# Kernel tuning notes

Hardware: AMD Instinct MI355X
Metric: run time of the kernel (lower is better)

Reference implementation:

```python
import jax, jax.numpy as jnp
import numpy as np

N_NODES = 50000
D_IN = 128
HIDDEN = 128
UNITS_DENSE = 256
N_EDGES = 600000
N_PRED = 200000
N_SEL = 300000


def setup_inputs() -> dict:
    key = jax.random.key(0)
    ks = jax.random.split(key, 12)
    node_state = jax.random.normal(ks[0], (N_NODES, D_IN), jnp.float32)
    edge_index = jax.random.randint(ks[1], (2, N_EDGES), 0, N_NODES, jnp.int32)
    out_edges = jax.random.randint(ks[2], (2, N_PRED), 0, N_NODES, jnp.int32)
    set_idx = jnp.sort(jax.random.randint(ks[3], (N_SEL,), 0, 2 * N_PRED, jnp.int32))
    # Glorot-ish scaled weights
    W1 = jax.random.normal(ks[4], (D_IN, HIDDEN), jnp.float32) / np.float32(np.sqrt(D_IN))
    b1 = jnp.zeros((HIDDEN,), jnp.float32)
    W2 = jax.random.normal(ks[5], (HIDDEN, HIDDEN), jnp.float32) / np.float32(np.sqrt(HIDDEN))
    b2 = jnp.zeros((HIDDEN,), jnp.float32)
    dense_W = jax.random.normal(ks[6], (2 * 0 + HIDDEN, UNITS_DENSE), jnp.float32) / np.float32(np.sqrt(HIDDEN))
    dense_b = jnp.zeros((UNITS_DENSE,), jnp.float32)
    out_W = jax.random.normal(ks[7], (UNITS_DENSE, 2), jnp.float32) / np.float32(np.sqrt(UNITS_DENSE))
    out_b = jnp.zeros((2,), jnp.float32)
    return {
        "node_state": node_state, "edge_index": edge_index, "out_edges": out_edges,
        "set_idx": set_idx, "W1": W1, "b1": b1, "W2": W2, "b2": b2,
        "dense_W": dense_W, "dense_b": dense_b, "out_W": out_W, "out_b": out_b,
    }


def _graph_conv(h, src, dst, W, b):
    """DGL GraphConv, norm='both', no activation: D_in^{-1/2} A D_out^{-1/2} H W + b."""
    n = h.shape[0]
    ones = jnp.ones(src.shape[0], h.dtype)
    deg_out = jnp.clip(jax.ops.segment_sum(ones, src, num_segments=n), 1.0)  # [N]
    deg_in = jnp.clip(jax.ops.segment_sum(ones, dst, num_segments=n), 1.0)   # [N]
    h = (h * jax.lax.rsqrt(deg_out)[:, None]) @ W                            # [N, H]
    agg = jax.ops.segment_sum(h[src], dst, num_segments=n)                   # [N, H]
    return agg * jax.lax.rsqrt(deg_in)[:, None] + b


def reference(node_state, edge_index, out_edges, set_idx,
              W1, b1, W2, b2, dense_W, dense_b, out_W, out_b):
    src, dst = edge_index[0], edge_index[1]
    h = _graph_conv(node_state, src, dst, W1, b1)
    h = _graph_conv(h, src, dst, W2, b2)
    # concat along axis=0 as in the original: [2*E_pred, H]
    edge_state = jnp.concatenate([h[out_edges[0]], h[out_edges[1]]], axis=0)
    # boolean_mask replaced by equivalent gather of selected (True) rows
    edge_state_set = edge_state[set_idx]                                      # [N_SEL, H]
    hidden = jax.nn.relu(edge_state_set @ dense_W + dense_b)
    return jax.nn.softmax(hidden @ out_W + out_b, axis=-1)
```

## Files before the change

### kernel.cpp

```cpp
#include <hip/hip_runtime.h>

#define NN 50000
#define DD 128
#define NE 600000
#define NP 200000
#define NS 300000
#define NU 256
#define NBH 64
#define EPB 9375
#define NW 12500
#define NB64 782

typedef __attribute__((ext_vector_type(8))) short short8;
typedef __attribute__((ext_vector_type(4))) float floatx4;

__device__ inline float bf2f(unsigned int u16) {
    unsigned int x = u16 << 16;
    float f; __builtin_memcpy(&f, &x, 4); return f;
}
__device__ inline unsigned short f2bf(float f) {
    unsigned int x; __builtin_memcpy(&x, &f, 4);
    unsigned int lsb = (x >> 16) & 1u;
    x += 0x7fffu + lsb;
    return (unsigned short)(x >> 16);
}

__global__ __launch_bounds__(256) void k_hist(const int* __restrict__ ei,
                                              unsigned int* __restrict__ P) {
    __shared__ unsigned int hw[NW];
    int b = blockIdx.x, half = blockIdx.y, tid = threadIdx.x;
    for (int w = tid; w < NW; w += 256) hw[w] = 0;
    __syncthreads();
    const int* src = ei + (size_t)half * NE;
    int e0 = b * EPB, e1 = min(e0 + EPB, NE);
    for (int e = e0 + tid; e < e1; e += 256) {
        int s = src[e];
        atomicAdd(&hw[s >> 2], 1u << ((s & 3) * 8));
    }
    __syncthreads();
    unsigned int* Pb = P + ((size_t)half * NBH + b) * NW;
    for (int w = tid; w < NW; w += 256) Pb[w] = hw[w];
}

__global__ void k_reduce_cast(const unsigned int* __restrict__ P, int* __restrict__ deg_in,
                              float* __restrict__ r,
                              const float* __restrict__ W1, const float* __restrict__ W2,
                              const float* __restrict__ dW, unsigned short* __restrict__ BT1,
                              unsigned short* __restrict__ BT2, unsigned short* __restrict__ BTd) {
    int gid = blockIdx.x * 256 + threadIdx.x;
    if (gid < 2 * NW) {
        int half = (gid >= NW);
        int wl = gid - half * NW;
        const unsigned int* Ph = P + (size_t)half * NBH * NW + wl;
        int c0 = 0, c1 = 0, c2 = 0, c3 = 0;
        for (int b = 0; b < NBH; ++b) {
            unsigned int v = Ph[(size_t)b * NW];
            c0 += v & 0xff; c1 += (v >> 8) & 0xff; c2 += (v >> 16) & 0xff; c3 += v >> 24;
        }
        int nb = wl * 4;
        if (half) {
            int4 d = {c0, c1, c2, c3};
            *(int4*)(deg_in + nb) = d;
        }
        float4 rr = {rsqrtf((float)max(c0, 1)), rsqrtf((float)max(c1, 1)),
                     rsqrtf((float)max(c2, 1)), rsqrtf((float)max(c3, 1))};
        *(float4*)(r + (size_t)half * NN + nb) = rr;
    }
    {
        int t = gid;
        if (t < 16384) { int rr = t >> 7, cc = t & 127; BT1[cc * 128 + rr] = f2bf(W1[t]); }
        else if (t < 32768) { int t2 = t - 16384; int rr = t2 >> 7, cc = t2 & 127; BT2[cc * 128 + rr] = f2bf(W2[t2]); }
        else if (t < 65536) { int t2 = t - 32768; int rr = t2 >> 8, cc = t2 & 255; BTd[cc * 128 + rr] = f2bf(dW[t2]); }
    }
}

__global__ __launch_bounds__(1024) void k_scan(const int* __restrict__ deg_in,
                                               int* __restrict__ row_ptr) {
    __shared__ int wsum[16];
    __shared__ int woff[16];
    __shared__ int carry_s;
    __shared__ int total_s;
    int tid = threadIdx.x, lane = tid & 63, w = tid >> 6;
    if (tid == 0) carry_s = 0;
    __syncthreads();
    for (int wb = 0; wb < NW; wb += 1024) {
        int i4 = wb + tid;
        int4 v = {0, 0, 0, 0};
        if (i4 < NW) v = *(const int4*)(deg_in + i4 * 4);
        int t0 = v.x, t1 = t0 + v.y, t2 = t1 + v.z, tot = t2 + v.w;
        int x = tot;
#pragma unroll
        for (int off = 1; off < 64; off <<= 1) {
            int y = __shfl_up(x, off);
            if (lane >= off) x += y;
        }
        if (lane == 63) wsum[w] = x;
        __syncthreads();
        if (w == 0 && lane < 16) {
            int s = wsum[lane];
            int xs = s;
#pragma unroll
            for (int off = 1; off < 16; off <<= 1) {
                int y = __shfl_up(xs, off);
                if (lane >= off) xs += y;
            }
            woff[lane] = xs - s;
            if (lane == 15) total_s = xs;
        }
        __syncthreads();
        if (i4 < NW) {
            int base = carry_s + woff[w] + x - tot;
            int4 o = {base, base + t0, base + t1, base + t2};
            *(int4*)(row_ptr + i4 * 4) = o;
        }
        __syncthreads();
        if (tid == 0) carry_s += total_s;
        __syncthreads();
    }
    if (tid == 0) row_ptr[NN] = NE;
}

__global__ void k_colscan(const unsigned int* __restrict__ Pin,
                          unsigned char* __restrict__ baseb) {
    int n = blockIdx.x * 256 + threadIdx.x;
    if (n >= NN) return;
    int wl = n >> 2, sh = (n & 3) * 8;
    int run = 0;
    for (int b = 0; b < NBH; ++b) {
        baseb[(size_t)b * NN + n] = (unsigned char)run;
        run += (Pin[(size_t)b * NW + wl] >> sh) & 0xff;
    }
}

__global__ __launch_bounds__(256) void k_bucket2(const int* __restrict__ ei,
                                                 const int* __restrict__ row_ptr,
                                                 const unsigned char* __restrict__ baseb,
                                                 int* __restrict__ col) {
    __shared__ unsigned int cw[NW];
    int b = blockIdx.x, tid = threadIdx.x;
    for (int w = tid; w < NW; w += 256) cw[w] = 0;
    __syncthreads();
    const unsigned char* bt = baseb + (size_t)b * NN;
    int e0 = b * EPB, e1 = min(e0 + EPB, NE);
    for (int e = e0 + tid; e < e1; e += 256) {
        int s = ei[e], d = ei[NE + e];
        int sh = (d & 3) * 8;
        unsigned int old = atomicAdd(&cw[d >> 2], 1u << sh);
        int local = (old >> sh) & 0xff;
        col[row_ptr[d] + (int)bt[d] + local] = s;
    }
}

template <bool ABF>
__global__ __launch_bounds__(256) void k_gemm_bf(const void* __restrict__ Ap,
                                                 const float* __restrict__ rs,
                                                 const unsigned short* __restrict__ BT,
                                                 unsigned short* __restrict__ Cm) {
    __shared__ unsigned short As[64][136];
    __shared__ unsigned short Bs[128][136];
    int tid = threadIdx.x, lane = tid & 63, wave = tid >> 6;
    int quad = lane >> 4, l16 = lane & 15;
    int row0 = blockIdx.x * 64;

    if (ABF) {
        const unsigned short* A = (const unsigned short*)Ap;
#pragma unroll
        for (int p = 0; p < 4; ++p) {
            int fid = tid + p * 256;
            int r = fid >> 4, c = fid & 15;
            int gr = row0 + r; if (gr > NN - 1) gr = NN - 1;
            *(uint4*)&As[r][c * 8] = *(const uint4*)(A + (size_t)gr * DD + c * 8);
        }
    } else {
        const float* A = (const float*)Ap;
#pragma unroll
        for (int p = 0; p < 8; ++p) {
            int fid = tid + p * 256;
            int r = fid >> 5, c = fid & 31;
            int gr = row0 + r; if (gr > NN - 1) gr = NN - 1;
            float4 v = *(const float4*)(A + (size_t)gr * DD + c * 4);
            ushort4 u;
            u.x = f2bf(v.x); u.y = f2bf(v.y); u.z = f2bf(v.z); u.w = f2bf(v.w);
            *(ushort4*)&As[r][c * 4] = u;
        }
    }
#pragma unroll
    for (int p = 0; p < 8; ++p) {
        int fid = tid + p * 256;
        int r = fid >> 4, c = fid & 15;
        *(uint4*)&Bs[r][c * 8] = *(const uint4*)(BT + (size_t)r * DD + c * 8);
    }
    __syncthreads();

    short8 af[4];
#pragma unroll
    for (int ks = 0; ks < 4; ++ks)
        af[ks] = *(const short8*)&As[wave * 16 + l16][ks * 32 + quad * 8];
    floatx4 acc[8];
#pragma unroll
    for (int nt = 0; nt < 8; ++nt) acc[nt] = (floatx4){0.f, 0.f, 0.f, 0.f};
#pragma unroll
    for (int ks = 0; ks < 4; ++ks) {
#pragma unroll
        for (int nt = 0; nt < 8; ++nt) {
            short8 bf = *(const short8*)&Bs[nt * 16 + l16][ks * 32 + quad * 8];
            acc[nt] = __builtin_amdgcn_mfma_f32_16x16x32_bf16(af[ks], bf, acc[nt], 0, 0, 0);
        }
    }
    int rbase = row0 + wave * 16 + quad * 4;
#pragma unroll
    for (int r = 0; r < 4; ++r) {
        int gr = rbase + r;
        if (gr < NN) {
            float s = rs[gr];
#pragma unroll
            for (int nt = 0; nt < 8; ++nt)
                Cm[(size_t)gr * DD + nt * 16 + l16] = f2bf(acc[nt][r] * s);
        }
    }
}

__global__ __launch_bounds__(256) void k_aggregate(const unsigned short* __restrict__ T,
                                                   const int* __restrict__ row_ptr,
                                                   const int* __restrict__ col,
                                                   const float* __restrict__ r_in,
                                                   const float* __restrict__ b,
                                                   unsigned short* __restrict__ H) {
    int wave = threadIdx.x >> 6, lane = threadIdx.x & 63;
    int sub = lane >> 4, l16 = lane & 15;
    int node = blockIdx.x * 16 + wave * 4 + sub;
    if (node >= NN) return;
    int beg = row_ptr[node], end = row_ptr[node + 1];
    float a0 = 0.f, a1 = 0.f, a2 = 0.f, a3 = 0.f, a4 = 0.f, a5 = 0.f, a6 = 0.f, a7 = 0.f;
    for (int base = beg; base < end; base += 16) {
        int m = end - base; if (m > 16) m = 16;
        int myidx = (l16 < m) ? col[base + l16] : 0;
        int j = 0;
        for (; j + 4 <= m; j += 4) {
            int s0 = __shfl(myidx, (sub << 4) | j);
            int s1 = __shfl(myidx, (sub << 4) | (j + 1));
            int s2 = __shfl(myidx, (sub << 4) | (j + 2));
            int s3 = __shfl(myidx, (sub << 4) | (j + 3));
            uint4 v0 = *(const uint4*)(T + (size_t)s0 * DD + l16 * 8);
            uint4 v1 = *(const uint4*)(T + (size_t)s1 * DD + l16 * 8);
            uint4 v2 = *(const uint4*)(T + (size_t)s2 * DD + l16 * 8);
            uint4 v3 = *(const uint4*)(T + (size_t)s3 * DD + l16 * 8);
            a0 += bf2f(v0.x & 0xffff) + bf2f(v1.x & 0xffff) + bf2f(v2.x & 0xffff) + bf2f(v3.x & 0xffff);
            a1 += bf2f(v0.x >> 16)    + bf2f(v1.x >> 16)    + bf2f(v2.x >> 16)    + bf2f(v3.x >> 16);
            a2 += bf2f(v0.y & 0xffff) + bf2f(v1.y & 0xffff) + bf2f(v2.y & 0xffff) + bf2f(v3.y & 0xffff);
            a3 += bf2f(v0.y >> 16)    + bf2f(v1.y >> 16)    + bf2f(v2.y >> 16)    + bf2f(v3.y >> 16);
            a4 += bf2f(v0.z & 0xffff) + bf2f(v1.z & 0xffff) + bf2f(v2.z & 0xffff) + bf2f(v3.z & 0xffff);
            a5 += bf2f(v0.z >> 16)    + bf2f(v1.z >> 16)    + bf2f(v2.z >> 16)    + bf2f(v3.z >> 16);
            a6 += bf2f(v0.w & 0xffff) + bf2f(v1.w & 0xffff) + bf2f(v2.w & 0xffff) + bf2f(v3.w & 0xffff);
            a7 += bf2f(v0.w >> 16)    + bf2f(v1.w >> 16)    + bf2f(v2.w >> 16)    + bf2f(v3.w >> 16);
        }
        for (; j < m; ++j) {
            int s0 = __shfl(myidx, (sub << 4) | j);
            uint4 v0 = *(const uint4*)(T + (size_t)s0 * DD + l16 * 8);
            a0 += bf2f(v0.x & 0xffff); a1 += bf2f(v0.x >> 16);
            a2 += bf2f(v0.y & 0xffff); a3 += bf2f(v0.y >> 16);
            a4 += bf2f(v0.z & 0xffff); a5 += bf2f(v0.z >> 16);
            a6 += bf2f(v0.w & 0xffff); a7 += bf2f(v0.w >> 16);
        }
    }
    float rv = r_in[node];
    float4 bl = *(const float4*)(b + l16 * 8);
    float4 bh = *(const float4*)(b + l16 * 8 + 4);
    uint4 w;
    w.x = (unsigned int)f2bf(a0 * rv + bl.x) | ((unsigned int)f2bf(a1 * rv + bl.y) << 16);
    w.y = (unsigned int)f2bf(a2 * rv + bl.z) | ((unsigned int)f2bf(a3 * rv + bl.w) << 16);
    w.z = (unsigned int)f2bf(a4 * rv + bh.x) | ((unsigned int)f2bf(a5 * rv + bh.y) << 16);
    w.w = (unsigned int)f2bf(a6 * rv + bh.z) | ((unsigned int)f2bf(a7 * rv + bh.w) << 16);
    *(uint4*)(H + (size_t)node * DD + l16 * 8) = w;
}

__global__ __launch_bounds__(256) void k_mlp_mfma(const unsigned short* __restrict__ H2,
                                                  const unsigned short* __restrict__ BTd,
                                                  const float* __restrict__ db,
                                                  const float* __restrict__ oW,
                                                  const float* __restrict__ ob,
                                                  float* __restrict__ P) {
    __shared__ unsigned short As[64][136];
    __shared__ unsigned short Bs[128][136];
    int tid = threadIdx.x, lane = tid & 63, wave = tid >> 6;
    int quad = lane >> 4, l16 = lane & 15;
    int row0 = blockIdx.x * 64;
#pragma unroll
    for (int p = 0; p < 4; ++p) {
        int fid = tid + p * 256;
        int r = fid >> 4, c = fid & 15;
        int gr = row0 + r; if (gr > NN - 1) gr = NN - 1;
        *(uint4*)&As[r][c * 8] = *(const uint4*)(H2 + (size_t)gr * DD + c * 8);
    }
    short8 af[4];
    floatx4 acc[16];
#pragma unroll
    for (int i = 0; i < 16; ++i) acc[i] = (floatx4){0.f, 0.f, 0.f, 0.f};

    for (int ch = 0; ch < 2; ++ch) {
        __syncthreads();
#pragma unroll
        for (int p = 0; p < 8; ++p) {
            int fid = tid + p * 256;
            int r = fid >> 4, c = fid & 15;
            *(uint4*)&Bs[r][c * 8] = *(const uint4*)(BTd + (size_t)(ch * 128 + r) * DD + c * 8);
        }
        __syncthreads();
        if (ch == 0) {
#pragma unroll
            for (int ks = 0; ks < 4; ++ks)
                af[ks] = *(const short8*)&As[wave * 16 + l16][ks * 32 + quad * 8];
        }
#pragma unroll
        for (int ks = 0; ks < 4; ++ks) {
#pragma unroll
            for (int nt = 0; nt < 8; ++nt) {
                short8 bf = *(const short8*)&Bs[nt * 16 + l16][ks * 32 + quad * 8];
                acc[ch * 8 + nt] =
                    __builtin_amdgcn_mfma_f32_16x16x32_bf16(af[ks], bf, acc[ch * 8 + nt], 0, 0, 0);
            }
        }
    }
    int rbase = row0 + wave * 16 + quad * 4;
#pragma unroll
    for (int r = 0; r < 4; ++r) {
        float p0 = 0.f, p1 = 0.f;
#pragma unroll
        for (int ch = 0; ch < 2; ++ch) {
#pragma unroll
            for (int nt = 0; nt < 8; ++nt) {
                int colc = ch * 128 + nt * 16 + l16;
                float h = acc[ch * 8 + nt][r] + db[colc];
                h = fmaxf(h, 0.f);
                p0 += h * oW[2 * colc];
                p1 += h * oW[2 * colc + 1];
            }
        }
#pragma unroll
        for (int m = 8; m >= 1; m >>= 1) {
            p0 += __shfl_xor(p0, m, 16);
            p1 += __shfl_xor(p1, m, 16);
        }
        if (l16 == 0) {
            int gr = rbase + r;
            if (gr < NN) {
                float l0 = p0 + ob[0], l1 = p1 + ob[1];
                float mx = fmaxf(l0, l1);
                float e0 = __expf(l0 - mx), e1 = __expf(l1 - mx);
                float inv = 1.f / (e0 + e1);
                float2 pr = {e0 * inv, e1 * inv};
                *(float2*)(P + 2 * gr) = pr;
            }
        }
    }
}

__global__ void k_gather(const int* __restrict__ sidx, const int* __restrict__ oe,
                         const float* __restrict__ P, float* __restrict__ out) {
    int i = blockIdx.x * 256 + threadIdx.x;
    if (i >= NS) return;
    int node = oe[sidx[i]];
    float2 v = *(const float2*)(P + 2 * node);
    *(float2*)(out + 2 * i) = v;
}

extern "C" void kernel_launch(void* const* d_in, const int* in_sizes, int n_in,
                              void* d_out, int out_size, void* d_ws, size_t ws_size,
                              hipStream_t stream) {
    const float* node_state = (const float*)d_in[0];
    const int* ei   = (const int*)d_in[1];
    const int* oe   = (const int*)d_in[2];
    const int* sidx = (const int*)d_in[3];
    const float* W1 = (const float*)d_in[4];
    const float* b1 = (const float*)d_in[5];
    const float* W2 = (const float*)d_in[6];
    const float* b2 = (const float*)d_in[7];
    const float* dW = (const float*)d_in[8];
    const float* db = (const float*)d_in[9];
    const float* oW = (const float*)d_in[10];
    const float* ob = (const float*)d_in[11];
    float* out = (float*)d_out;

    char* ws = (char*)d_ws;
    size_t off = 0;
    auto carve = [&](size_t bytes) -> char* {
        char* p = ws + off;
        off = (off + bytes + 255) & ~(size_t)255;
        return p;
    };
    int*   deg_in  = (int*)carve((size_t)NN * 4);
    float* r       = (float*)carve((size_t)2 * NN * 4);
    int*   row_ptr = (int*)carve((size_t)(NN + 1) * 4);
    int*   col     = (int*)carve((size_t)NE * 4);
    unsigned int* P_hist = (unsigned int*)carve((size_t)2 * NBH * NW * 4);
    unsigned char* baseb = (unsigned char*)carve((size_t)NBH * NN);
    unsigned short* t   = (unsigned short*)carve((size_t)NN * DD * 2);
    unsigned short* h   = (unsigned short*)carve((size_t)NN * DD * 2);
    unsigned short* BT1 = (unsigned short*)carve((size_t)DD * DD * 2);
    unsigned short* BT2 = (unsigned short*)carve((size_t)DD * DD * 2);
    unsigned short* BTd = (unsigned short*)carve((size_t)DD * NU * 2);
    float* P = (float*)t;

    float* r_out = r;
    float* r_in  = r + NN;

    k_hist<<<dim3(NBH, 2), 256, 0, stream>>>(ei, P_hist);
    k_reduce_cast<<<256, 256, 0, stream>>>(P_hist, deg_in, r, W1, W2, dW, BT1, BT2, BTd);
    k_scan<<<1, 1024, 0, stream>>>(deg_in, row_ptr);
    k_colscan<<<(NN + 255) / 256, 256, 0, stream>>>(P_hist + (size_t)NBH * NW, baseb);
    k_bucket2<<<NBH, 256, 0, stream>>>(ei, row_ptr, baseb, col);

    k_gemm_bf<false><<<NB64, 256, 0, stream>>>(node_state, r_out, BT1, t);
    k_aggregate<<<(NN + 15) / 16, 256, 0, stream>>>(t, row_ptr, col, r_in, b1, h);

    k_gemm_bf<true><<<NB64, 256, 0, stream>>>(h, r_out, BT2, t);
    k_aggregate<<<(NN + 15) / 16, 256, 0, stream>>>(t, row_ptr, col, r_in, b2, h);

    k_mlp_mfma<<<NB64, 256, 0, stream>>>(h, BTd, db, oW, ob, P);
    k_gather<<<(NS + 255) / 256, 256, 0, stream>>>(sidx, oe, P, out);
}
```

Baseline: 258.7 us.

## Fuse degree reduce, prefix scan and column scan into one decoupled-lookback kernel

Merges the degree reduction/weight cast, the single-block row_ptr scan and the per-bucket column scan into a single kernel. The scan becomes a multi-block decoupled-lookback scan over 49 blocks, using a status array that k_hist zeroes, instead of a serial 1024-thread loop in one block. This removes two kernel launches and the serial single-block scan. In exchange it relies on spin-waiting across blocks, which assumes earlier blocks make forward progress, and it drops the deg_in buffer.

```diff
diff --git a/kernel.cpp b/kernel.cpp
--- a/kernel.cpp
+++ b/kernel.cpp
@@ -10,6 +10,7 @@
 #define EPB 9375
 #define NW 12500
 #define NB64 782
+#define NSCAN 49
 
 typedef __attribute__((ext_vector_type(8))) short short8;
 typedef __attribute__((ext_vector_type(4))) float floatx4;
@@ -26,9 +27,11 @@
 }
 
 __global__ __launch_bounds__(256) void k_hist(const int* __restrict__ ei,
-                                              unsigned int* __restrict__ P) {
+                                              unsigned int* __restrict__ P,
+                                              unsigned long long* __restrict__ status) {
     __shared__ unsigned int hw[NW];
     int b = blockIdx.x, half = blockIdx.y, tid = threadIdx.x;
+    if (b == 0 && half == 0 && tid < 64) status[tid] = 0ull;
     for (int w = tid; w < NW; w += 256) hw[w] = 0;
     __syncthreads();
     const int* src = ei + (size_t)half * NE;
@@ -42,52 +45,53 @@
     for (int w = tid; w < NW; w += 256) Pb[w] = hw[w];
 }
 
-__global__ void k_reduce_cast(const unsigned int* __restrict__ P, int* __restrict__ deg_in,
-                              float* __restrict__ r,
-                              const float* __restrict__ W1, const float* __restrict__ W2,
-                              const float* __restrict__ dW, unsigned short* __restrict__ BT1,
-                              unsigned short* __restrict__ BT2, unsigned short* __restrict__ BTd) {
-    int gid = blockIdx.x * 256 + threadIdx.x;
-    if (gid < 2 * NW) {
-        int half = (gid >= NW);
-        int wl = gid - half * NW;
-        const unsigned int* Ph = P + (size_t)half * NBH * NW + wl;
+__global__ __launch_bounds__(256) void k_mid(
+    const unsigned int* __restrict__ P_hist, float* __restrict__ r,
+    const float* __restrict__ W1, const float* __restrict__ W2, const float* __restrict__ dW,
+    unsigned short* __restrict__ BT1, unsigned short* __restrict__ BT2,
+    unsigned short* __restrict__ BTd,
+    int* __restrict__ row_ptr, unsigned char* __restrict__ baseb,
+    unsigned long long* __restrict__ status)
+{
+    int b = blockIdx.x, tid = threadIdx.x, lane = tid & 63, w = tid >> 6;
+    int gid = b * 256 + tid;
+
+    int4 v = {0, 0, 0, 0};
+    if (gid < NW) {
+        const unsigned int* Ph = P_hist + (size_t)NBH * NW + gid;
         int c0 = 0, c1 = 0, c2 = 0, c3 = 0;
-        for (int b = 0; b < NBH; ++b) {
-            unsigned int v = Ph[(size_t)b * NW];
-            c0 += v & 0xff; c1 += (v >> 8) & 0xff; c2 += (v >> 16) & 0xff; c3 += v >> 24;
-        }
-        int nb = wl * 4;
-        if (half) {
-            int4 d = {c0, c1, c2, c3};
-            *(int4*)(deg_in + nb) = d;
-        }
+        for (int b2 = 0; b2 < NBH; ++b2) {
+            unsigned int x = Ph[(size_t)b2 * NW];
+            c0 += x & 0xff; c1 += (x >> 8) & 0xff; c2 += (x >> 16) & 0xff; c3 += x >> 24;
+        }
+        v = (int4){c0, c1, c2, c3};
         float4 rr = {rsqrtf((float)max(c0, 1)), rsqrtf((float)max(c1, 1)),
                      rsqrtf((float)max(c2, 1)), rsqrtf((float)max(c3, 1))};
-        *(float4*)(r + (size_t)half * NN + nb) = rr;
-    }
+        *(float4*)(r + NN + gid * 4) = rr;
+    } else if (gid < 2 * NW) {
+        int wl = gid - NW;
+        const unsigned int* Ph = P_hist + wl;
+        int c0 = 0, c1 = 0, c2 = 0, c3 = 0;
+        for (int b2 = 0; b2 < NBH; ++b2) {
+            unsigned int x = Ph[(size_t)b2 * NW];
+            c0 += x & 0xff; c1 += (x >> 8) & 0xff; c2 += (x >> 16) & 0xff; c3 += x >> 24;
+        }
+        float4 rr = {rsqrtf((float)max(c0, 1)), rsqrtf((float)max(c1, 1)),
+                     rsqrtf((float)max(c2, 1)), rsqrtf((float)max(c3, 1))};
+        *(float4*)(r + wl * 4) = rr;
+    }
+
     {
         int t = gid;
         if (t < 16384) { int rr = t >> 7, cc = t & 127; BT1[cc * 128 + rr] = f2bf(W1[t]); }
         else if (t < 32768) { int t2 = t - 16384; int rr = t2 >> 7, cc = t2 & 127; BT2[cc * 128 + rr] = f2bf(W2[t2]); }
         else if (t < 65536) { int t2 = t - 32768; int rr = t2 >> 8, cc = t2 & 255; BTd[cc * 128 + rr] = f2bf(dW[t2]); }
     }
-}
-
-__global__ __launch_bounds__(1024) void k_scan(const int* __restrict__ deg_in,
-                                               int* __restrict__ row_ptr) {
-    __shared__ int wsum[16];
-    __shared__ int woff[16];
-    __shared__ int carry_s;
-    __shared__ int total_s;
-    int tid = threadIdx.x, lane = tid & 63, w = tid >> 6;
-    if (tid == 0) carry_s = 0;
-    __syncthreads();
-    for (int wb = 0; wb < NW; wb += 1024) {
-        int i4 = wb + tid;
-        int4 v = {0, 0, 0, 0};
-        if (i4 < NW) v = *(const int4*)(deg_in + i4 * 4);
-        int t0 = v.x, t1 = t0 + v.y, t2 = t1 + v.z, tot = t2 + v.w;
+
+    if (b < NSCAN) {
+        __shared__ int wsum[4];
+        __shared__ long long sbase;
+        int tot = v.x + v.y + v.z + v.w;
         int x = tot;
 #pragma unroll
         for (int off = 1; off < 64; off <<= 1) {
@@ -96,39 +100,52 @@
         }
         if (lane == 63) wsum[w] = x;
         __syncthreads();
-        if (w == 0 && lane < 16) {
-            int s = wsum[lane];
-            int xs = s;
-#pragma unroll
-            for (int off = 1; off < 16; off <<= 1) {
-                int y = __shfl_up(xs, off);
-                if (lane >= off) xs += y;
+        int woff = 0;
+#pragma unroll
+        for (int i = 0; i < 4; ++i) if (i < w) woff += wsum[i];
+        if (tid == 0) {
+            int btot = wsum[0] + wsum[1] + wsum[2] + wsum[3];
+            if (b == 0) {
+                sbase = 0;
+                __threadfence();
+                atomicExch(&status[0], (2ull << 62) | (unsigned long long)btot);
+            } else {
+                __threadfence();
+                atomicExch(&status[b], (1ull << 62) | (unsigned long long)btot);
+                long long run = 0; int j = b - 1;
+                while (true) {
+                    unsigned long long s;
+                    do { s = atomicAdd(&status[j], 0ull); } while (s == 0ull);
+                    run += (long long)(s & 0x3fffffffffffffffull);
+                    if ((s >> 62) == 2ull) break;
+                    --j;
+                }
+                sbase = run;
+                __threadfence();
+                atomicExch(&status[b], (2ull << 62) | (unsigned long long)(run + btot));
             }
-            woff[lane] = xs - s;
-            if (lane == 15) total_s = xs;
         }
         __syncthreads();
-        if (i4 < NW) {
-            int base = carry_s + woff[w] + x - tot;
-            int4 o = {base, base + t0, base + t1, base + t2};
-            *(int4*)(row_ptr + i4 * 4) = o;
-        }
-        __syncthreads();
-        if (tid == 0) carry_s += total_s;
-        __syncthreads();
-    }
-    if (tid == 0) row_ptr[NN] = NE;
-}
-
-__global__ void k_colscan(const unsigned int* __restrict__ Pin,
-                          unsigned char* __restrict__ baseb) {
-    int n = blockIdx.x * 256 + threadIdx.x;
-    if (n >= NN) return;
-    int wl = n >> 2, sh = (n & 3) * 8;
-    int run = 0;
-    for (int b = 0; b < NBH; ++b) {
-        baseb[(size_t)b * NN + n] = (unsigned char)run;
-        run += (Pin[(size_t)b * NW + wl] >> sh) & 0xff;
+        if (gid < NW) {
+            int base = (int)sbase + woff + (x - tot);
+            int4 o = {base, base + v.x, base + v.x + v.y, base + v.x + v.y + v.z};
+            *(int4*)(row_ptr + gid * 4) = o;
+        }
+        if (b == 0 && tid == 0) row_ptr[NN] = NE;
+    }
+
+    int cb = b - NSCAN;
+    if (cb >= 0 && cb < 196) {
+        int n = cb * 256 + tid;
+        if (n < NN) {
+            int wl = n >> 2, sh = (n & 3) * 8;
+            int run = 0;
+            const unsigned int* Pd = P_hist + (size_t)NBH * NW;
+            for (int b2 = 0; b2 < NBH; ++b2) {
+                baseb[(size_t)b2 * NN + n] = (unsigned char)run;
+                run += (Pd[(size_t)b2 * NW + wl] >> sh) & 0xff;
+            }
+        }
     }
 }
 
@@ -388,12 +405,12 @@
         off = (off + bytes + 255) & ~(size_t)255;
         return p;
     };
-    int*   deg_in  = (int*)carve((size_t)NN * 4);
     float* r       = (float*)carve((size_t)2 * NN * 4);
     int*   row_ptr = (int*)carve((size_t)(NN + 1) * 4);
     int*   col     = (int*)carve((size_t)NE * 4);
     unsigned int* P_hist = (unsigned int*)carve((size_t)2 * NBH * NW * 4);
     unsigned char* baseb = (unsigned char*)carve((size_t)NBH * NN);
+    unsigned long long* status = (unsigned long long*)carve(64 * 8);
     unsigned short* t   = (unsigned short*)carve((size_t)NN * DD * 2);
     unsigned short* h   = (unsigned short*)carve((size_t)NN * DD * 2);
     unsigned short* BT1 = (unsigned short*)carve((size_t)DD * DD * 2);
@@ -404,10 +421,9 @@
     float* r_out = r;
     float* r_in  = r + NN;
 
-    k_hist<<<dim3(NBH, 2), 256, 0, stream>>>(ei, P_hist);
-    k_reduce_cast<<<256, 256, 0, stream>>>(P_hist, deg_in, r, W1, W2, dW, BT1, BT2, BTd);
-    k_scan<<<1, 1024, 0, stream>>>(deg_in, row_ptr);
-    k_colscan<<<(NN + 255) / 256, 256, 0, stream>>>(P_hist + (size_t)NBH * NW, baseb);
+    k_hist<<<dim3(NBH, 2), 256, 0, stream>>>(ei, P_hist, status);
+    k_mid<<<256, 256, 0, stream>>>(P_hist, r, W1, W2, dW, BT1, BT2, BTd,
+                                   row_ptr, baseb, status);
     k_bucket2<<<NBH, 256, 0, stream>>>(ei, row_ptr, baseb, col);
 
     k_gemm_bf<false><<<NB64, 256, 0, stream>>>(node_state, r_out, BT1, t);
```

Measured after the change: 248.3 us. -4.0%, faster.
